# Kernel optimization log

Hardware: AMD Instinct MI355X
Metric: run time of the kernel (lower is better)

## Reference

```python
import jax, jax.numpy as jnp
import numpy as np

N = 8192
E = 262144
NFEAT = 200
NHID = 128
NOUT = 16
CLUSTERS = (10, 5)


def _layernorm(x, g, b, eps=1e-5):
    mu = jnp.mean(x, axis=-1, keepdims=True)
    var = jnp.var(x, axis=-1, keepdims=True)
    return (x - mu) / jnp.sqrt(var + eps) * g + b


def _gumbel_softmax_hard(logits, g, tau=1.0):
    # straight-through gumbel softmax (hard=True), dim=1
    y = jax.nn.softmax((logits + g) / tau, axis=1)
    hard = jax.nn.one_hot(jnp.argmax(y, axis=1), y.shape[1], dtype=y.dtype)
    return hard + y - jax.lax.stop_gradient(y)


def _row_normalize(x, eps=1e-12):
    n = jnp.linalg.norm(x, axis=1, keepdims=True)
    return x / jnp.maximum(n, eps)


def setup_inputs() -> dict:
    key = jax.random.key(0)
    ks = jax.random.split(key, 20)
    u0 = jax.random.uniform(ks[3], (N, CLUSTERS[0]), minval=1e-6, maxval=1.0 - 1e-6)
    u1 = jax.random.uniform(ks[4], (CLUSTERS[0], CLUSTERS[1]), minval=1e-6, maxval=1.0 - 1e-6)
    s = 0.05
    return {
        'x': jax.random.normal(ks[0], (N, NFEAT), dtype=jnp.float32),
        'edge_index': jax.random.randint(ks[1], (2, E), 0, N, dtype=jnp.int32),
        'edge_weight': jax.random.uniform(ks[2], (E,), dtype=jnp.float32),
        'gumbel0': -jnp.log(-jnp.log(u0)),
        'gumbel1': -jnp.log(-jnp.log(u1)),
        # GCN params (2 layers, layernorm)
        'Wg1': jax.random.normal(ks[5], (NHID, NFEAT)) * s,
        'bg1': jnp.zeros((NHID,)),
        'ln1_g': jnp.ones((NHID,)), 'ln1_b': jnp.zeros((NHID,)),
        'Wg2': jax.random.normal(ks[6], (NHID, NHID)) * s,
        'bg2': jnp.zeros((NHID,)),
        'ln2_g': jnp.ones((NHID,)), 'ln2_b': jnp.zeros((NHID,)),
        # per-level pool + encoder linears
        'pool0_W': jax.random.normal(ks[7], (CLUSTERS[0], NHID)) * s,
        'pool0_b': jnp.zeros((CLUSTERS[0],)),
        'pool1_W': jax.random.normal(ks[8], (CLUSTERS[1], NHID)) * s,
        'pool1_b': jnp.zeros((CLUSTERS[1],)),
        'enc0_W': jax.random.normal(ks[9], (NHID, NHID)) * s,
        'enc0_b': jnp.zeros((NHID,)),
        'enc1_W': jax.random.normal(ks[10], (NHID, NHID)) * s,
        'enc1_b': jnp.zeros((NHID,)),
        'fc_W': jax.random.normal(ks[11], (NOUT, 3 * NHID)) * s,
        'fc_b': jnp.zeros((NOUT,)),
    }


def reference(x, edge_index, edge_weight, gumbel0, gumbel1,
              Wg1, bg1, ln1_g, ln1_b, Wg2, bg2, ln2_g, ln2_b,
              pool0_W, pool0_b, pool1_W, pool1_b,
              enc0_W, enc0_b, enc1_W, enc1_b, fc_W, fc_b):
    src, dst = edge_index[0], edge_index[1]

    def agg(h):  # weighted neighbor sum: out[i] = sum_{e: dst_e=i} w_e * h[src_e]
        return jax.ops.segment_sum(h[src] * edge_weight[:, None], dst, num_segments=N)

    # bottom GCN encoder (2 layers, layernorm)
    h = agg(x) @ Wg1.T + bg1
    h = jax.nn.relu(_layernorm(h, ln1_g, ln1_b))
    h = agg(h) @ Wg2.T + bg2
    h = _layernorm(h, ln2_g, ln2_b)
    latent = jax.nn.relu(h)  # [N, nhid]
    all_latents = [latent]

    # dense adjacency (to_dense_adj)
    adj = jnp.zeros((N, N), dtype=x.dtype).at[src, dst].add(edge_weight)

    pools = [(pool0_W, pool0_b), (pool1_W, pool1_b)]
    encs = [(enc0_W, enc0_b), (enc1_W, enc1_b)]
    gumbels = [gumbel0, gumbel1]
    product = None
    for level in range(len(CLUSTERS)):
        pW, pb = pools[level]
        eW, eb = encs[level]
        assign = _gumbel_softmax_hard(latent @ pW.T + pb, gumbels[level])  # [n_l, K]
        product = assign if level == 0 else product @ assign  # [N, K]
        xc = _row_normalize(assign.T @ latent)  # [K, nhid]
        adj = assign.T @ adj @ assign  # [K, K]
        adj = adj / jnp.sum(adj + 1e-8)
        latent = jax.nn.relu((adj @ xc) @ eW.T + eb)  # [K, nhid]
        all_latents.append(product @ latent)  # [N, nhid]

    rep = jnp.concatenate(all_latents, axis=1)  # [N, 3*nhid]
    return rep @ fc_W.T + fc_b
```

## Files before the change

kernel.cpp:

```cpp
#include <hip/hip_runtime.h>

#define N_NODES 8192
#define N_EDGES 262144
#define NFEAT 200
#define NHID 128

template<int K>
__device__ __forceinline__ void gemm_body(const float* __restrict__ A,
                                          const float* __restrict__ W,
                                          float* __restrict__ C, int bid) {
    __shared__ float a_s[8 * K];
    int row0 = bid * 8;
    const float* Ab = A + (size_t)row0 * K;
    for (int idx = threadIdx.x; idx < 8 * K; idx += 128) a_s[idx] = Ab[idx];
    __syncthreads();
    int j = threadIdx.x;
    float acc[8] = {0.f, 0.f, 0.f, 0.f, 0.f, 0.f, 0.f, 0.f};
    const float4* W4 = (const float4*)(W + (size_t)j * K);
    for (int k4 = 0; k4 < K / 4; ++k4) {
        float4 w = W4[k4];
        int k = k4 * 4;
        #pragma unroll
        for (int r = 0; r < 8; ++r) {
            const float* ar = a_s + r * K + k;
            acc[r] += ar[0] * w.x + ar[1] * w.y + ar[2] * w.z + ar[3] * w.w;
        }
    }
    #pragma unroll
    for (int r = 0; r < 8; ++r) C[(size_t)(row0 + r) * 128 + j] = acc[r];
}

__global__ __launch_bounds__(128) void gemm1_hist(const float* __restrict__ A,
                                                  const float* __restrict__ W,
                                                  float* __restrict__ C,
                                                  const int* __restrict__ ei,
                                                  int* __restrict__ deg) {
    if (blockIdx.x < N_NODES / 8) {
        gemm_body<NFEAT>(A, W, C, blockIdx.x);
    } else {
        const int* dst = ei + N_EDGES;
        for (int e = (blockIdx.x - N_NODES / 8) * 128 + threadIdx.x; e < N_EDGES; e += 64 * 128)
            atomicAdd(&deg[dst[e]], 1);
    }
}

__global__ __launch_bounds__(256) void scan_kernel(const int* __restrict__ deg,
                                                   int* __restrict__ row_start,
                                                   int* __restrict__ cursor) {
    __shared__ int part[256];
    __shared__ int partx[257];
    int tid = threadIdx.x;
    int base = tid * 32;
    int s = 0;
    for (int i = 0; i < 32; ++i) s += deg[base + i];
    part[tid] = s;
    __syncthreads();
    if (tid == 0) {
        int run = 0;
        for (int i = 0; i < 256; ++i) { partx[i] = run; run += part[i]; }
        partx[256] = run;
    }
    __syncthreads();
    int run = partx[tid];
    for (int i = 0; i < 32; ++i) {
        row_start[base + i] = run;
        cursor[base + i] = run;
        run += deg[base + i];
    }
    if (tid == 255) row_start[N_NODES] = run;
}

__global__ __launch_bounds__(256) void scatter_kernel(const int* __restrict__ ei,
                                                      const float* __restrict__ ew,
                                                      int* __restrict__ cursor,
                                                      int2* __restrict__ esort, int E) {
    int e = blockIdx.x * blockDim.x + threadIdx.x;
    if (e < E) {
        int d = ei[E + e];
        int pos = atomicAdd(&cursor[d], 1);
        esort[pos] = make_int2(ei[e], __float_as_int(ew[e]));
    }
}

__device__ __forceinline__ float2 csr_gather(const int* __restrict__ row_start,
                                             const int2* __restrict__ esort,
                                             const float* __restrict__ H,
                                             int row, int lane) {
    int s0 = row_start[row], s1 = row_start[row + 1];
    float ax0 = 0.f, ay0 = 0.f, ax1 = 0.f, ay1 = 0.f;
    float ax2 = 0.f, ay2 = 0.f, ax3 = 0.f, ay3 = 0.f;
    int e = s0;
    for (; e + 3 < s1; e += 4) {
        int2 p0 = esort[e], p1 = esort[e + 1], p2 = esort[e + 2], p3 = esort[e + 3];
        float2 v0 = *(const float2*)(H + (size_t)p0.x * 128 + lane * 2);
        float2 v1 = *(const float2*)(H + (size_t)p1.x * 128 + lane * 2);
        float2 v2 = *(const float2*)(H + (size_t)p2.x * 128 + lane * 2);
        float2 v3 = *(const float2*)(H + (size_t)p3.x * 128 + lane * 2);
        float w0 = __int_as_float(p0.y), w1 = __int_as_float(p1.y);
        float w2 = __int_as_float(p2.y), w3 = __int_as_float(p3.y);
        ax0 += w0 * v0.x; ay0 += w0 * v0.y;
        ax1 += w1 * v1.x; ay1 += w1 * v1.y;
        ax2 += w2 * v2.x; ay2 += w2 * v2.y;
        ax3 += w3 * v3.x; ay3 += w3 * v3.y;
    }
    for (; e < s1; ++e) {
        int2 p0 = esort[e];
        float2 v0 = *(const float2*)(H + (size_t)p0.x * 128 + lane * 2);
        float w0 = __int_as_float(p0.y);
        ax0 += w0 * v0.x; ay0 += w0 * v0.y;
    }
    return make_float2((ax0 + ax1) + (ax2 + ax3), (ay0 + ay1) + (ay2 + ay3));
}

__device__ __forceinline__ float2 ln_relu(float vx, float vy, int lane,
                                          const float* __restrict__ bias,
                                          const float* __restrict__ g,
                                          const float* __restrict__ b) {
    float2 bs = *(const float2*)(bias + lane * 2);
    vx += bs.x; vy += bs.y;
    float s = vx + vy, ss = vx * vx + vy * vy;
    for (int off = 32; off; off >>= 1) {
        s += __shfl_xor(s, off, 64);
        ss += __shfl_xor(ss, off, 64);
    }
    float mu = s * (1.f / 128.f);
    float var = ss * (1.f / 128.f) - mu * mu;
    float rs = rsqrtf(var + 1e-5f);
    float2 gg = *(const float2*)(g + lane * 2);
    float2 bb = *(const float2*)(b + lane * 2);
    return make_float2(fmaxf((vx - mu) * rs * gg.x + bb.x, 0.f),
                       fmaxf((vy - mu) * rs * gg.y + bb.y, 0.f));
}

__global__ __launch_bounds__(256) void agg1_gemm2(const int* __restrict__ row_start,
                                                  const int2* __restrict__ esort,
                                                  const float* __restrict__ bufA,
                                                  const float* __restrict__ Wg2,
                                                  float* __restrict__ bufC,
                                                  const float* __restrict__ bias,
                                                  const float* __restrict__ g,
                                                  const float* __restrict__ b) {
    __shared__ float rows[4 * 128];
    int lane = threadIdx.x & 63, wid = threadIdx.x >> 6;
    int row0 = blockIdx.x * 4;
    {
        float2 a = csr_gather(row_start, esort, bufA, row0 + wid, lane);
        float2 y = ln_relu(a.x, a.y, lane, bias, g, b);
        rows[wid * 128 + lane * 2] = y.x;
        rows[wid * 128 + lane * 2 + 1] = y.y;
    }
    __syncthreads();
    int j = threadIdx.x & 127, rh = threadIdx.x >> 7;
    const float4* wp = (const float4*)(Wg2 + (size_t)j * 128);
    const float4* r0 = (const float4*)(rows + rh * 128);
    const float4* r1 = (const float4*)(rows + (rh + 2) * 128);
    float acc0 = 0.f, acc1 = 0.f;
    #pragma unroll 8
    for (int kk = 0; kk < 32; ++kk) {
        float4 w = wp[kk];
        float4 a0 = r0[kk], a1 = r1[kk];
        acc0 += a0.x * w.x + a0.y * w.y + a0.z * w.z + a0.w * w.w;
        acc1 += a1.x * w.x + a1.y * w.y + a1.z * w.z + a1.w * w.w;
    }
    bufC[(size_t)(row0 + rh) * 128 + j] = acc0;
    bufC[(size_t)(row0 + rh + 2) * 128 + j] = acc1;
}

__global__ __launch_bounds__(256) void agg2_pool0(const int* __restrict__ row_start,
                                                  const int2* __restrict__ esort,
                                                  const float* __restrict__ bufC,
                                                  float* __restrict__ latent,
                                                  const float* __restrict__ bias,
                                                  const float* __restrict__ g,
                                                  const float* __restrict__ b,
                                                  const float* __restrict__ p0W,
                                                  const float* __restrict__ p0b,
                                                  const float* __restrict__ gum,
                                                  int* __restrict__ c0,
                                                  float* __restrict__ partials) {
    __shared__ float Ws[1280];
    __shared__ float accs[1280];
    __shared__ float bsh[10];
    for (int i = threadIdx.x; i < 1280; i += 256) { Ws[i] = p0W[i]; accs[i] = 0.f; }
    if (threadIdx.x < 10) bsh[threadIdx.x] = p0b[threadIdx.x];
    __syncthreads();
    int lane = threadIdx.x & 63, wid = threadIdx.x >> 6;
    int base = blockIdx.x * 16;
    for (int rr = 0; rr < 4; ++rr) {
        int row = base + rr * 4 + wid;
        float2 a = csr_gather(row_start, esort, bufC, row, lane);
        float2 y = ln_relu(a.x, a.y, lane, bias, g, b);
        *(float2*)(latent + (size_t)row * 128 + lane * 2) = y;
        float pk[10];
        #pragma unroll
        for (int k = 0; k < 10; ++k)
            pk[k] = y.x * Ws[k * 128 + lane * 2] + y.y * Ws[k * 128 + lane * 2 + 1];
        for (int off = 32; off; off >>= 1) {
            #pragma unroll
            for (int k = 0; k < 10; ++k) pk[k] += __shfl_xor(pk[k], off, 64);
        }
        const float* gr = gum + (size_t)row * 10;
        int best = 0;
        float bv = pk[0] + bsh[0] + gr[0];
        #pragma unroll
        for (int k = 1; k < 10; ++k) {
            float z = pk[k] + bsh[k] + gr[k];
            if (z > bv) { bv = z; best = k; }
        }
        if (lane == 0) c0[row] = best;
        atomicAdd(&accs[best * 128 + lane * 2], y.x);
        atomicAdd(&accs[best * 128 + lane * 2 + 1], y.y);
    }
    __syncthreads();
    for (int i = threadIdx.x; i < 1280; i += 256)
        partials[(size_t)blockIdx.x * 1280 + i] = accs[i];
}

__global__ __launch_bounds__(256) void adj_xc0(const int* __restrict__ ei,
                                               const float* __restrict__ ew,
                                               const int* __restrict__ c0,
                                               float* __restrict__ A0,
                                               const float* __restrict__ partials,
                                               float* __restrict__ xc0, int E) {
    if (blockIdx.x < 256) {
        __shared__ float As[100];
        for (int i = threadIdx.x; i < 100; i += 256) As[i] = 0.f;
        __syncthreads();
        for (int e = blockIdx.x * 256 + threadIdx.x; e < E; e += 256 * 256) {
            int a = c0[ei[e]], b = c0[ei[E + e]];
            atomicAdd(&As[a * 10 + b], ew[e]);
        }
        __syncthreads();
        for (int i = threadIdx.x; i < 100; i += 256) atomicAdd(&A0[i], As[i]);
    } else {
        int k = blockIdx.x - 256;
        int d = threadIdx.x & 127, half = threadIdx.x >> 7;
        float s0 = 0.f, s1 = 0.f, s2 = 0.f, s3 = 0.f;
        for (int b = half * 256; b < half * 256 + 256; b += 4) {
            s0 += partials[(size_t)(b    ) * 1280 + k * 128 + d];
            s1 += partials[(size_t)(b + 1) * 1280 + k * 128 + d];
            s2 += partials[(size_t)(b + 2) * 1280 + k * 128 + d];
            s3 += partials[(size_t)(b + 3) * 1280 + k * 128 + d];
        }
        __shared__ float sm[256];
        sm[threadIdx.x] = (s0 + s1) + (s2 + s3);
        __syncthreads();
        if (threadIdx.x < 128) xc0[k * 128 + d] = sm[threadIdx.x] + sm[threadIdx.x + 128];
    }
}

__global__ __launch_bounds__(256) void small_kernel(const float* __restrict__ xc0,
                                                    const float* __restrict__ A0,
                                                    const float* __restrict__ gum1,
                                                    const float* __restrict__ p1W,
                                                    const float* __restrict__ p1b,
                                                    const float* __restrict__ e0W,
                                                    const float* __restrict__ e0b,
                                                    const float* __restrict__ e1W,
                                                    const float* __restrict__ e1b,
                                                    const float* __restrict__ fcW,
                                                    const float* __restrict__ fcb,
                                                    float* __restrict__ tbl) {
    __shared__ float xc0n[10 * 128];
    __shared__ float adj0[100];
    __shared__ float m0[10 * 128];
    __shared__ float l1[10 * 128];
    __shared__ float xc1n[5 * 128];
    __shared__ float l2[5 * 128];
    __shared__ float A1[25];
    __shared__ int c1[10];
    __shared__ float red[4];

    int tid = threadIdx.x;
    int wid = tid >> 6, lane = tid & 63;

    for (int r = wid; r < 10; r += 4) {
        float2 v = *(const float2*)(xc0 + r * 128 + lane * 2);
        float ss = v.x * v.x + v.y * v.y;
        for (int off = 32; off; off >>= 1) ss += __shfl_xor(ss, off, 64);
        float sc = 1.f / fmaxf(sqrtf(ss), 1e-12f);
        xc0n[r * 128 + lane * 2] = v.x * sc;
        xc0n[r * 128 + lane * 2 + 1] = v.y * sc;
    }
    __syncthreads();
    if (tid == 0) {
        float s = 0.f;
        for (int i = 0; i < 100; ++i) s += A0[i];
        red[0] = s + 1e-6f;
    }
    __syncthreads();
    if (tid < 100) adj0[tid] = A0[tid] / red[0];
    __syncthreads();
    for (int idx = tid; idx < 1280; idx += 256) {
        int r = idx >> 7, d = idx & 127;
        float acc = 0.f;
        #pragma unroll
        for (int a = 0; a < 10; ++a) acc += adj0[r * 10 + a] * xc0n[a * 128 + d];
        m0[idx] = acc;
    }
    __syncthreads();
    for (int idx = tid; idx < 1280; idx += 256) {
        int r = idx >> 7, d = idx & 127;
        float acc = e0b[d];
        const float* wrow = e0W + d * 128;
        for (int k = 0; k < 128; ++k) acc += m0[r * 128 + k] * wrow[k];
        l1[idx] = fmaxf(acc, 0.f);
    }
    __syncthreads();
    if (tid < 10) {
        int best = 0;
        float bv = -1e30f;
        for (int j = 0; j < 5; ++j) {
            float acc = p1b[j] + gum1[tid * 5 + j];
            const float* wrow = p1W + j * 128;
            for (int k = 0; k < 128; ++k) acc += l1[tid * 128 + k] * wrow[k];
            if (acc > bv) { bv = acc; best = j; }
        }
        c1[tid] = best;
    }
    __syncthreads();
    for (int idx = tid; idx < 640; idx += 256) {
        int m = idx >> 7, d = idx & 127;
        float acc = 0.f;
        #pragma unroll
        for (int k = 0; k < 10; ++k)
            if (c1[k] == m) acc += l1[k * 128 + d];
        xc1n[idx] = acc;
    }
    __syncthreads();
    for (int r = wid; r < 5; r += 4) {
        float2 v = *(const float2*)(xc1n + r * 128 + lane * 2);
        float ss = v.x * v.x + v.y * v.y;
        for (int off = 32; off; off >>= 1) ss += __shfl_xor(ss, off, 64);
        float sc = 1.f / fmaxf(sqrtf(ss), 1e-12f);
        xc1n[r * 128 + lane * 2] = v.x * sc;
        xc1n[r * 128 + lane * 2 + 1] = v.y * sc;
    }
    __syncthreads();
    if (tid < 25) {
        int m = tid / 5, n = tid % 5;
        float acc = 0.f;
        for (int a = 0; a < 10; ++a)
            for (int b = 0; b < 10; ++b)
                if (c1[a] == m && c1[b] == n) acc += adj0[a * 10 + b];
        A1[tid] = acc;
    }
    __syncthreads();
    if (tid == 0) {
        float s = 0.f;
        for (int i = 0; i < 25; ++i) s += A1[i];
        red[1] = s + 25e-8f;
    }
    __syncthreads();
    float den1 = red[1];
    for (int idx = tid; idx < 640; idx += 256) {
        int r = idx >> 7, d = idx & 127;
        float acc = 0.f;
        #pragma unroll
        for (int a = 0; a < 5; ++a) acc += A1[r * 5 + a] * xc1n[a * 128 + d];
        m0[idx] = acc / den1;
    }
    __syncthreads();
    for (int idx = tid; idx < 640; idx += 256) {
        int r = idx >> 7, d = idx & 127;
        float acc = e1b[d];
        const float* wrow = e1W + d * 128;
        for (int k = 0; k < 128; ++k) acc += m0[r * 128 + k] * wrow[k];
        l2[idx] = fmaxf(acc, 0.f);
    }
    __syncthreads();
    for (int idx = tid; idx < 160; idx += 256) {
        int k = idx >> 4, o = idx & 15;
        float acc = fcb[o];
        const float* fB = fcW + o * 384 + 128;
        const float* fC = fcW + o * 384 + 256;
        const float* a1 = l1 + k * 128;
        const float* a2 = l2 + c1[k] * 128;
        for (int d = 0; d < 128; ++d) acc += a1[d] * fB[d] + a2[d] * fC[d];
        tbl[idx] = acc;
    }
}

__global__ __launch_bounds__(256) void out_kernel(const float* __restrict__ latent,
                                                  const int* __restrict__ c0,
                                                  const float* __restrict__ tbl,
                                                  const float* __restrict__ fcW,
                                                  float* __restrict__ out) {
    __shared__ float fA[16 * 128];
    __shared__ float ts[160];
    for (int i = threadIdx.x; i < 2048; i += 256) {
        int o = i >> 7, d = i & 127;
        fA[i] = fcW[o * 384 + d];
    }
    for (int i = threadIdx.x; i < 160; i += 256) ts[i] = tbl[i];
    __syncthreads();
    int lane = threadIdx.x & 63;
    int sub = lane & 7;
    int row = blockIdx.x * 32 + (threadIdx.x >> 6) * 8 + (lane >> 3);
    const float4* lp = (const float4*)(latent + (size_t)row * 128 + sub * 16);
    float4 x0 = lp[0], x1 = lp[1], x2 = lp[2], x3 = lp[3];
    float p[16];
    #pragma unroll
    for (int o = 0; o < 16; ++o) {
        const float4* fo = (const float4*)(fA + o * 128 + sub * 16);
        float4 w0 = fo[0], w1 = fo[1], w2 = fo[2], w3 = fo[3];
        float a = x0.x * w0.x + x0.y * w0.y + x0.z * w0.z + x0.w * w0.w;
        a += x1.x * w1.x + x1.y * w1.y + x1.z * w1.z + x1.w * w1.w;
        a += x2.x * w2.x + x2.y * w2.y + x2.z * w2.z + x2.w * w2.w;
        a += x3.x * w3.x + x3.y * w3.y + x3.z * w3.z + x3.w * w3.w;
        p[o] = a;
    }
    #pragma unroll
    for (int off = 1; off < 8; off <<= 1) {
        #pragma unroll
        for (int o = 0; o < 16; ++o) p[o] += __shfl_xor(p[o], off, 64);
    }
    int c = c0[row];
    float2 r = make_float2(p[2 * sub] + ts[c * 16 + 2 * sub],
                           p[2 * sub + 1] + ts[c * 16 + 2 * sub + 1]);
    *(float2*)(out + (size_t)row * 16 + 2 * sub) = r;
}

extern "C" void kernel_launch(void* const* d_in, const int* in_sizes, int n_in,
                              void* d_out, int out_size, void* d_ws, size_t ws_size,
                              hipStream_t stream) {
    const float* x    = (const float*)d_in[0];
    const int*   ei   = (const int*)d_in[1];
    const float* ew   = (const float*)d_in[2];
    const float* g0   = (const float*)d_in[3];
    const float* g1   = (const float*)d_in[4];
    const float* Wg1  = (const float*)d_in[5];
    const float* bg1  = (const float*)d_in[6];
    const float* ln1g = (const float*)d_in[7];
    const float* ln1b = (const float*)d_in[8];
    const float* Wg2  = (const float*)d_in[9];
    const float* bg2  = (const float*)d_in[10];
    const float* ln2g = (const float*)d_in[11];
    const float* ln2b = (const float*)d_in[12];
    const float* p0W  = (const float*)d_in[13];
    const float* p0b  = (const float*)d_in[14];
    const float* p1W  = (const float*)d_in[15];
    const float* p1b  = (const float*)d_in[16];
    const float* e0W  = (const float*)d_in[17];
    const float* e0b  = (const float*)d_in[18];
    const float* e1W  = (const float*)d_in[19];
    const float* e1b  = (const float*)d_in[20];
    const float* fcW  = (const float*)d_in[21];
    const float* fcb  = (const float*)d_in[22];
    float* out = (float*)d_out;

    float* ws   = (float*)d_ws;
    float* bufA = ws;
    float* bufB = bufA + (size_t)N_NODES * 128;
    float* bufC = bufB + (size_t)N_NODES * 128;
    int*   c0   = (int*)(bufC + (size_t)N_NODES * 128);
    float* xc0  = (float*)(c0 + N_NODES);
    float* tbl  = xc0 + 1280;
    int*   deg  = (int*)(tbl + 160);
    float* A0   = (float*)(deg + N_NODES);
    int*   row_start = (int*)(A0 + 100);
    int*   cursor    = row_start + N_NODES + 2;
    int2*  esort     = (int2*)(cursor + N_NODES);
    float* partials  = bufA;

    hipMemsetAsync(deg, 0, (N_NODES + 100) * sizeof(int), stream);

    gemm1_hist<<<N_NODES / 8 + 64, 128, 0, stream>>>(x, Wg1, bufA, ei, deg);
    scan_kernel<<<1, 256, 0, stream>>>(deg, row_start, cursor);
    scatter_kernel<<<N_EDGES / 256, 256, 0, stream>>>(ei, ew, cursor, esort, N_EDGES);

    agg1_gemm2<<<N_NODES / 4, 256, 0, stream>>>(row_start, esort, bufA, Wg2, bufC,
                                                bg1, ln1g, ln1b);

    agg2_pool0<<<512, 256, 0, stream>>>(row_start, esort, bufC, bufB,
                                        bg2, ln2g, ln2b, p0W, p0b, g0, c0, partials);

    adj_xc0<<<266, 256, 0, stream>>>(ei, ew, c0, A0, partials, xc0, N_EDGES);

    small_kernel<<<1, 256, 0, stream>>>(xc0, A0, g1, p1W, p1b, e0W, e0b, e1W, e1b,
                                        fcW, fcb, tbl);

    out_kernel<<<256, 256, 0, stream>>>(bufB, c0, tbl, fcW, out);
}
```

Before: 207.9 us.

## Split agg1 and GEMM2 into separate kernels and wave-cooperative edge metadata loads

The fused aggregate+LayerNorm+GEMM kernel is split into a standalone CSR aggregate/LayerNorm kernel writing to an intermediate buffer, followed by a separate 8-row-tiled GEMM kernel reusing the existing gemm body. The CSR gather now loads up to 64 edge records cooperatively, one per lane, and broadcasts source index and weight via shuffles instead of every lane loading the same records. This aims to cut redundant metadata loads and give the GEMM better weight reuse. In exchange it adds a kernel launch and a full N×128 intermediate write and read.

```diff
diff --git a/kernel.cpp b/kernel.cpp
--- a/kernel.cpp
+++ b/kernel.cpp
@@ -28,6 +28,13 @@
     }
     #pragma unroll
     for (int r = 0; r < 8; ++r) C[(size_t)(row0 + r) * 128 + j] = acc[r];
+}
+
+template<int K>
+__global__ __launch_bounds__(128) void gemm_rows(const float* __restrict__ A,
+                                                 const float* __restrict__ W,
+                                                 float* __restrict__ C) {
+    gemm_body<K>(A, W, C, blockIdx.x);
 }
 
 __global__ __launch_bounds__(128) void gemm1_hist(const float* __restrict__ A,
@@ -89,25 +96,36 @@
     int s0 = row_start[row], s1 = row_start[row + 1];
     float ax0 = 0.f, ay0 = 0.f, ax1 = 0.f, ay1 = 0.f;
     float ax2 = 0.f, ay2 = 0.f, ax3 = 0.f, ay3 = 0.f;
-    int e = s0;
-    for (; e + 3 < s1; e += 4) {
-        int2 p0 = esort[e], p1 = esort[e + 1], p2 = esort[e + 2], p3 = esort[e + 3];
-        float2 v0 = *(const float2*)(H + (size_t)p0.x * 128 + lane * 2);
-        float2 v1 = *(const float2*)(H + (size_t)p1.x * 128 + lane * 2);
-        float2 v2 = *(const float2*)(H + (size_t)p2.x * 128 + lane * 2);
-        float2 v3 = *(const float2*)(H + (size_t)p3.x * 128 + lane * 2);
-        float w0 = __int_as_float(p0.y), w1 = __int_as_float(p1.y);
-        float w2 = __int_as_float(p2.y), w3 = __int_as_float(p3.y);
-        ax0 += w0 * v0.x; ay0 += w0 * v0.y;
-        ax1 += w1 * v1.x; ay1 += w1 * v1.y;
-        ax2 += w2 * v2.x; ay2 += w2 * v2.y;
-        ax3 += w3 * v3.x; ay3 += w3 * v3.y;
-    }
-    for (; e < s1; ++e) {
-        int2 p0 = esort[e];
-        float2 v0 = *(const float2*)(H + (size_t)p0.x * 128 + lane * 2);
-        float w0 = __int_as_float(p0.y);
-        ax0 += w0 * v0.x; ay0 += w0 * v0.y;
+    for (int base = s0; base < s1; base += 64) {
+        int n = s1 - base;
+        if (n > 64) n = 64;
+        int2 meta = make_int2(0, 0);
+        if (lane < n) meta = esort[base + lane];
+        int k = 0;
+        for (; k + 3 < n; k += 4) {
+            int sA = __shfl(meta.x, k, 64);
+            int sB = __shfl(meta.x, k + 1, 64);
+            int sC = __shfl(meta.x, k + 2, 64);
+            int sD = __shfl(meta.x, k + 3, 64);
+            float wA = __int_as_float(__shfl(meta.y, k, 64));
+            float wB = __int_as_float(__shfl(meta.y, k + 1, 64));
+            float wC = __int_as_float(__shfl(meta.y, k + 2, 64));
+            float wD = __int_as_float(__shfl(meta.y, k + 3, 64));
+            float2 vA = *(const float2*)(H + (size_t)sA * 128 + lane * 2);
+            float2 vB = *(const float2*)(H + (size_t)sB * 128 + lane * 2);
+            float2 vC = *(const float2*)(H + (size_t)sC * 128 + lane * 2);
+            float2 vD = *(const float2*)(H + (size_t)sD * 128 + lane * 2);
+            ax0 += wA * vA.x; ay0 += wA * vA.y;
+            ax1 += wB * vB.x; ay1 += wB * vB.y;
+            ax2 += wC * vC.x; ay2 += wC * vC.y;
+            ax3 += wD * vD.x; ay3 += wD * vD.y;
+        }
+        for (; k < n; ++k) {
+            int sA = __shfl(meta.x, k, 64);
+            float wA = __int_as_float(__shfl(meta.y, k, 64));
+            float2 vA = *(const float2*)(H + (size_t)sA * 128 + lane * 2);
+            ax0 += wA * vA.x; ay0 += wA * vA.y;
+        }
     }
     return make_float2((ax0 + ax1) + (ax2 + ax3), (ay0 + ay1) + (ay2 + ay3));
 }
@@ -132,38 +150,18 @@
                        fmaxf((vy - mu) * rs * gg.y + bb.y, 0.f));
 }
 
-__global__ __launch_bounds__(256) void agg1_gemm2(const int* __restrict__ row_start,
+__global__ __launch_bounds__(256) void agg_ln_csr(const int* __restrict__ row_start,
                                                   const int2* __restrict__ esort,
-                                                  const float* __restrict__ bufA,
-                                                  const float* __restrict__ Wg2,
-                                                  float* __restrict__ bufC,
+                                                  const float* __restrict__ H,
+                                                  float* __restrict__ out,
                                                   const float* __restrict__ bias,
                                                   const float* __restrict__ g,
                                                   const float* __restrict__ b) {
-    __shared__ float rows[4 * 128];
-    int lane = threadIdx.x & 63, wid = threadIdx.x >> 6;
-    int row0 = blockIdx.x * 4;
-    {
-        float2 a = csr_gather(row_start, esort, bufA, row0 + wid, lane);
-        float2 y = ln_relu(a.x, a.y, lane, bias, g, b);
-        rows[wid * 128 + lane * 2] = y.x;
-        rows[wid * 128 + lane * 2 + 1] = y.y;
-    }
-    __syncthreads();
-    int j = threadIdx.x & 127, rh = threadIdx.x >> 7;
-    const float4* wp = (const float4*)(Wg2 + (size_t)j * 128);
-    const float4* r0 = (const float4*)(rows + rh * 128);
-    const float4* r1 = (const float4*)(rows + (rh + 2) * 128);
-    float acc0 = 0.f, acc1 = 0.f;
-    #pragma unroll 8
-    for (int kk = 0; kk < 32; ++kk) {
-        float4 w = wp[kk];
-        float4 a0 = r0[kk], a1 = r1[kk];
-        acc0 += a0.x * w.x + a0.y * w.y + a0.z * w.z + a0.w * w.w;
-        acc1 += a1.x * w.x + a1.y * w.y + a1.z * w.z + a1.w * w.w;
-    }
-    bufC[(size_t)(row0 + rh) * 128 + j] = acc0;
-    bufC[(size_t)(row0 + rh + 2) * 128 + j] = acc1;
+    int wave = (blockIdx.x * blockDim.x + threadIdx.x) >> 6;
+    int lane = threadIdx.x & 63;
+    float2 a = csr_gather(row_start, esort, H, wave, lane);
+    float2 y = ln_relu(a.x, a.y, lane, bias, g, b);
+    *(float2*)(out + (size_t)wave * 128 + lane * 2) = y;
 }
 
 __global__ __launch_bounds__(256) void agg2_pool0(const int* __restrict__ row_start,
@@ -469,8 +467,9 @@
     scan_kernel<<<1, 256, 0, stream>>>(deg, row_start, cursor);
     scatter_kernel<<<N_EDGES / 256, 256, 0, stream>>>(ei, ew, cursor, esort, N_EDGES);
 
-    agg1_gemm2<<<N_NODES / 4, 256, 0, stream>>>(row_start, esort, bufA, Wg2, bufC,
+    agg_ln_csr<<<N_NODES / 4, 256, 0, stream>>>(row_start, esort, bufA, bufB,
                                                 bg1, ln1g, ln1b);
+    gemm_rows<NHID><<<N_NODES / 8, 128, 0, stream>>>(bufB, Wg2, bufC);
 
     agg2_pool0<<<512, 256, 0, stream>>>(row_start, esort, bufC, bufB,
                                         bg2, ln2g, ln2b, p0W, p0b, g0, c0, partials);
```

New measurement: 186.1 us. 1.12x faster.
